# Performance work log

Hardware: AMD Instinct MI355X
Metric: run time of the kernel (lower is better)

## Reference

```python
import jax, jax.numpy as jnp
import numpy as np

B, A, T, C = 8, 16, 512, 256
H = 8
DH = C // H
HID = 4 * C


def setup_inputs() -> dict:
    key = jax.random.key(0)
    ks = jax.random.split(key, 16)
    s = 0.02
    return {
        "x": jax.random.normal(ks[0], (B, A, T, C), jnp.float32),
        "ln1_w": jnp.ones((C,), jnp.float32),
        "ln1_b": jnp.zeros((C,), jnp.float32),
        "qkv_w": jax.random.normal(ks[1], (C, 3 * C), jnp.float32) * s,
        "qkv_b": jnp.zeros((3 * C,), jnp.float32),
        "proj_w": jax.random.normal(ks[2], (C, C), jnp.float32) * s,
        "proj_b": jnp.zeros((C,), jnp.float32),
        "ln2_w": jnp.ones((C,), jnp.float32),
        "ln2_b": jnp.zeros((C,), jnp.float32),
        "fc_w": jax.random.normal(ks[3], (C, HID), jnp.float32) * s,
        "fc_b": jnp.zeros((HID,), jnp.float32),
        "fc2_w": jax.random.normal(ks[4], (HID, C), jnp.float32) * s,
        "fc2_b": jnp.zeros((C,), jnp.float32),
    }


def _layernorm(x, w, b, eps=1e-5):
    mu = jnp.mean(x, axis=-1, keepdims=True)
    var = jnp.var(x, axis=-1, keepdims=True)
    return (x - mu) * jax.lax.rsqrt(var + eps) * w + b


def reference(x, ln1_w, ln1_b, qkv_w, qkv_b, proj_w, proj_b,
              ln2_w, ln2_b, fc_w, fc_b, fc2_w, fc2_b):
    # pre-LN block; note: residuals branch off the *normalized* tensor,
    # exactly as in the source forward().
    xn = _layernorm(x, ln1_w, ln1_b)                       # (B,A,T,C)

    qkv = xn @ qkv_w + qkv_b                               # (B,A,T,3C)
    q, k, v = jnp.split(qkv, 3, axis=-1)
    # (B,A,T,C) -> (B,A,H,T,Dh)
    def heads(t):
        return t.reshape(B, A, T, H, DH).transpose(0, 1, 3, 2, 4)
    q, k, v = heads(q), heads(k), heads(v)

    att = jnp.einsum('bahtd,bahsd->bahts', q, k) / np.sqrt(DH).astype(np.float32)
    att = jax.nn.softmax(att, axis=-1)                     # (B,A,H,T,T)
    y = jnp.einsum('bahts,bahsd->bahtd', att, v)
    y = y.transpose(0, 1, 3, 2, 4).reshape(B, A, T, C)
    y = y @ proj_w + proj_b

    x2 = xn + y
    x2n = _layernorm(x2, ln2_w, ln2_b)
    h = jax.nn.gelu(x2n @ fc_w + fc_b, approximate=False)
    m = h @ fc2_w + fc2_b
    return x2n + m
```

## Files before the change

kernel.cpp:

```cpp
#include <hip/hip_runtime.h>

typedef unsigned short u16;
typedef __attribute__((ext_vector_type(8))) short s16x8;
typedef __attribute__((ext_vector_type(4))) float f32x4;

#define MFMA_BF16(a,b,c) __builtin_amdgcn_mfma_f32_16x16x32_bf16((a),(b),(c),0,0,0)

#define GLL(gp, lp) __builtin_amdgcn_global_load_lds( \
    (const __attribute__((address_space(1))) void*)(gp), \
    (__attribute__((address_space(3))) void*)(lp), 16, 0, 0)

#define PIPE_WAIT_BAR(N) do { \
  asm volatile("s_waitcnt vmcnt(" #N ")" ::: "memory"); \
  __builtin_amdgcn_sched_barrier(0); \
  __builtin_amdgcn_s_barrier(); \
  __builtin_amdgcn_sched_barrier(0); \
} while (0)

#define PIPE_BAR() do { \
  asm volatile("" ::: "memory"); \
  __builtin_amdgcn_sched_barrier(0); \
  __builtin_amdgcn_s_barrier(); \
  __builtin_amdgcn_sched_barrier(0); \
} while (0)

__device__ __forceinline__ float b2f(u16 s){
  union { unsigned u; float f; } v; v.u = ((unsigned)s) << 16; return v.f;
}
__device__ __forceinline__ u16 f2b(float x){
  union { float f; unsigned u; } v; v.f = x;
  unsigned u = v.u;
  return (u16)((u + 0x7FFFu + ((u >> 16) & 1u)) >> 16);
}
__device__ __forceinline__ u16 f2b_trunc(float x){
  union { float f; unsigned u; } v; v.f = x;
  return (u16)(v.u >> 16);
}

__device__ __forceinline__ float gelu_fast(float v){
  float av = fabsf(v) * 0.70710678118654752f;
  float t  = __builtin_amdgcn_rcpf(1.0f + 0.3275911f * av);
  float p  = ((((1.061405429f * t - 1.453152027f) * t + 1.421413741f) * t
               - 0.284496736f) * t + 0.254829592f) * t;
  float erfa = 1.0f - p * __expf(-av * av);
  return 0.5f * v * (1.0f + copysignf(erfa, v));
}

__global__ __launch_bounds__(256) void wconv_all(
    const float* __restrict__ w0, u16* __restrict__ t0,
    const float* __restrict__ w1, u16* __restrict__ t1,
    const float* __restrict__ w2, u16* __restrict__ t2,
    const float* __restrict__ w3, u16* __restrict__ t3)
{
  int bid = blockIdx.x;
  const float* w; u16* t; int K, N, base;
  if (bid < 768)        { w = w0; t = t0; K = 256;  N = 768;  base = bid; }
  else if (bid < 1024)  { w = w1; t = t1; K = 256;  N = 256;  base = bid - 768; }
  else if (bid < 2048)  { w = w2; t = t2; K = 256;  N = 1024; base = bid - 1024; }
  else                  { w = w3; t = t3; K = 1024; N = 256;  base = bid - 2048; }
  int idx = base * 256 + threadIdx.x;
  if (idx >= K * N) return;
  int k = idx / N, n = idx - k * N;
  t[(size_t)n * K + k] = f2b(w[idx]);
}

__global__ __launch_bounds__(256) void ln_f32(const float* __restrict__ in,
    const float* __restrict__ gam, const float* __restrict__ bet, u16* __restrict__ out)
{
  int wv = threadIdx.x >> 6, lane = threadIdx.x & 63;
  size_t row = (size_t)blockIdx.x * 4 + wv;
  float4 u = *(const float4*)(in + row * 256 + lane * 4);
  float s  = u.x + u.y + u.z + u.w;
  float s2 = u.x*u.x + u.y*u.y + u.z*u.z + u.w*u.w;
  #pragma unroll
  for (int off = 32; off; off >>= 1){
    s  += __shfl_xor(s, off);
    s2 += __shfl_xor(s2, off);
  }
  float mean = s * (1.0f/256.0f);
  float var  = s2 * (1.0f/256.0f) - mean*mean;
  float rs   = rsqrtf(var + 1e-5f);
  int c = lane * 4;
  float4 g4 = *(const float4*)(gam + c);
  float4 b4 = *(const float4*)(bet + c);
  ushort4 o;
  o.x = f2b((u.x - mean)*rs*g4.x + b4.x);
  o.y = f2b((u.y - mean)*rs*g4.y + b4.y);
  o.z = f2b((u.z - mean)*rs*g4.z + b4.z);
  o.w = f2b((u.w - mean)*rs*g4.w + b4.w);
  *(ushort4*)(out + row * 256 + c) = o;
}

template<int EPI, int NT>
__global__ __launch_bounds__(256) void gemm128(
    const u16* __restrict__ A, const u16* __restrict__ Bt, const float* __restrict__ bias,
    const u16* __restrict__ res, void* __restrict__ o0v, u16* __restrict__ o1, u16* __restrict__ o2,
    int N, int K)
{
  __shared__ __align__(16) u16 lds[24576];
  int tid = threadIdx.x;
  int w = tid >> 6, lane = tid & 63;
  int quad = lane >> 4, c = lane & 15;
  int bid = blockIdx.x;
  int x = bid & 7, j = bid >> 3;
  int nt = j % NT, mt = (j / NT) * 8 + x;
  int wm = (w >> 1) * 64, wn = (w & 1) * 64;
  const u16* Abase = A + (size_t)mt * 128 * K;
  const u16* Bbase = Bt + (size_t)nt * 128 * K;
  int m0 = tid & 127, jj0 = tid >> 7;
  f32x4 zero = {0.f, 0.f, 0.f, 0.f};
  f32x4 acc[4][4];
  #pragma unroll
  for (int mi = 0; mi < 4; mi++)
    #pragma unroll
    for (int ni = 0; ni < 4; ni++) acc[mi][ni] = zero;

  auto stage = [&](int buf, int k0){
    u16* base = &lds[buf * 8192];
    GLL(Abase + (size_t)m0 * K + k0 + jj0 * 8,       &base[tid * 8]);
    GLL(Abase + (size_t)m0 * K + k0 + (jj0 + 2) * 8, &base[2048 + tid * 8]);
    GLL(Bbase + (size_t)m0 * K + k0 + jj0 * 8,       &base[4096 + tid * 8]);
    GLL(Bbase + (size_t)m0 * K + k0 + (jj0 + 2) * 8, &base[6144 + tid * 8]);
  };
  auto compute = [&](int cb){
    const u16* Lb = &lds[cb * 8192];
    s16x8 af[4], bfr[4];
    #pragma unroll
    for (int mi = 0; mi < 4; mi++)
      af[mi] = *(const s16x8*)&Lb[(quad * 128 + wm + mi * 16 + c) * 8];
    #pragma unroll
    for (int ni = 0; ni < 4; ni++)
      bfr[ni] = *(const s16x8*)&Lb[4096 + (quad * 128 + wn + ni * 16 + c) * 8];
    #pragma unroll
    for (int mi = 0; mi < 4; mi++)
      #pragma unroll
      for (int ni = 0; ni < 4; ni++)
        acc[mi][ni] = MFMA_BF16(af[mi], bfr[ni], acc[mi][ni]);
  };

  stage(0, 0); stage(1, 32); stage(2, 64);
  int cur = 0;
  int k0 = 0;
  for (; k0 + 96 < K; k0 += 32){
    PIPE_WAIT_BAR(8);
    compute(cur);
    PIPE_BAR();
    stage(cur, k0 + 96);
    cur = (cur == 2) ? 0 : cur + 1;
  }
  PIPE_WAIT_BAR(8); compute(cur); cur = (cur == 2) ? 0 : cur + 1;
  PIPE_WAIT_BAR(4); compute(cur); cur = (cur == 2) ? 0 : cur + 1;
  PIPE_WAIT_BAR(0); compute(cur);

  const int LS  = 132;
  int rr = tid >> 3;
  int c7 = tid & 7;

  #pragma unroll
  for (int ch = 0; ch < 4; ch++){
    __syncthreads();
    if ((w >> 1) == (ch >> 1)){
      #pragma unroll
      for (int mi2 = 0; mi2 < 2; mi2++){
        int mi = (ch & 1) * 2 + mi2;
        #pragma unroll
        for (int ni = 0; ni < 4; ni++){
          int col = wn + ni * 16 + c;
          float bv = bias[nt * 128 + col];
          #pragma unroll
          for (int r = 0; r < 4; r++){
            int cr = mi2 * 16 + quad * 4 + r;
            float vv = acc[mi][ni][r] + bv;
            if (EPI == 0){
              int gcol = nt * 128 + col;
              if ((gcol >> 8) == 0) vv *= 0.17677669529663687f;
              lds[cr * LS + col] = f2b(vv);
            }
          }
        }
      }
    }
    __syncthreads();
    int row = mt * 128 + ch * 32 + rr;
    #pragma unroll
    for (int jj2 = 0; jj2 < 2; jj2++){
      int colL = c7 * 8 + jj2 * 64;
      uint4 val = *(const uint4*)&lds[rr * LS + colL];
      if (EPI == 0){
        int gcol = nt * 128 + colL;
        int which = gcol >> 8, ccc = gcol & 255;
        int hh = ccc >> 5, d = ccc & 31;
        int ba = row >> 9, t = row & 511;
        size_t idx = (((size_t)(ba * 8 + hh)) * 512 + t) * 32 + d;
        u16* dst = (which == 0) ? (u16*)o0v : ((which == 1) ? o1 : o2);
        *(uint4*)(dst + idx) = val;
      } else {
        *(uint4*)((u16*)o0v + (size_t)row * N + nt * 128 + colL) = val;
      }
    }
  }
}

__global__ __launch_bounds__(256) void ffn_fused(
    const u16* __restrict__ x2n, const u16* __restrict__ fcT, const float* __restrict__ fcb,
    const u16* __restrict__ fc2T, const float* __restrict__ fc2b, float* __restrict__ out)
{
  __shared__ __align__(16) u16 lds[24576];
  int tid = threadIdx.x;
  int w = tid >> 6, lane = tid & 63;
  int quad = lane >> 4, c = lane & 15;
  int mt = blockIdx.x;
  const u16* Abase = x2n + (size_t)mt * 64 * 256;
  char* ldsc = (char*)lds;
  char* hl   = (char*)lds + 32768;

  #pragma unroll
  for (int i = 0; i < 8; i++){
    int ci = i * 256 + tid;
    int row = ci >> 5, slot = ci & 31;
    int glow = (slot * 16) ^ ((row & 7) << 4);
    GLL((const char*)Abase + row * 512 + glow, ldsc + ci * 16);
  }
  f32x4 zero = {0.f, 0.f, 0.f, 0.f};
  f32x4 acc2[4][4];
  #pragma unroll
  for (int mi = 0; mi < 4; mi++)
    #pragma unroll
    for (int ni = 0; ni < 4; ni++) acc2[mi][ni] = zero;
  PIPE_WAIT_BAR(0);

  for (int hc = 0; hc < 8; hc++){
    f32x4 acc1[4][2];
    #pragma unroll
    for (int mi = 0; mi < 4; mi++){ acc1[mi][0] = zero; acc1[mi][1] = zero; }
    #pragma unroll
    for (int ks = 0; ks < 8; ks++){
      s16x8 af[4], bf1[2];
      #pragma unroll
      for (int ni = 0; ni < 2; ni++){
        int n = hc * 128 + w * 32 + ni * 16 + c;
        bf1[ni] = *(const s16x8*)(fcT + (size_t)n * 256 + ks * 32 + quad * 8);
      }
      #pragma unroll
      for (int mi = 0; mi < 4; mi++){
        int row = mi * 16 + c;
        int kb = (ks * 64 + quad * 16) ^ ((row & 7) << 4);
        af[mi] = *(const s16x8*)(ldsc + row * 512 + kb);
      }
      #pragma unroll
      for (int mi = 0; mi < 4; mi++){
        acc1[mi][0] = MFMA_BF16(af[mi], bf1[0], acc1[mi][0]);
        acc1[mi][1] = MFMA_BF16(af[mi], bf1[1], acc1[mi][1]);
      }
    }
    __syncthreads();
    #pragma unroll
    for (int ni = 0; ni < 2; ni++){
      int colc = w * 32 + ni * 16 + c;
      float bv = fcb[hc * 128 + colc];
      #pragma unroll
      for (int mi = 0; mi < 4; mi++){
        #pragma unroll
        for (int r = 0; r < 4; r++){
          int row = mi * 16 + quad * 4 + r;
          int by = (colc * 2) ^ ((row & 15) << 4);
          *(u16*)(hl + row * 256 + by) = f2b(gelu_fast(acc1[mi][ni][r] + bv));
        }
      }
    }
    __syncthreads();
    #pragma unroll
    for (int ks = 0; ks < 4; ks++){
      s16x8 ha[4], bf2[4];
      #pragma unroll
      for (int ni = 0; ni < 4; ni++){
        int n = w * 64 + ni * 16 + c;
        bf2[ni] = *(const s16x8*)(fc2T + (size_t)n * 1024 + hc * 128 + ks * 32 + quad * 8);
      }
      #pragma unroll
      for (int mi = 0; mi < 4; mi++){
        int row = mi * 16 + c;
        int kb = (ks * 64 + quad * 16) ^ ((row & 15) << 4);
        ha[mi] = *(const s16x8*)(hl + row * 256 + kb);
      }
      #pragma unroll
      for (int mi = 0; mi < 4; mi++)
        #pragma unroll
        for (int ni = 0; ni < 4; ni++)
          acc2[mi][ni] = MFMA_BF16(ha[mi], bf2[ni], acc2[mi][ni]);
    }
  }

  #pragma unroll
  for (int ni = 0; ni < 4; ni++){
    int col = w * 64 + ni * 16 + c;
    float bv = fc2b[col];
    #pragma unroll
    for (int mi = 0; mi < 4; mi++){
      #pragma unroll
      for (int r = 0; r < 4; r++){
        int row = mi * 16 + quad * 4 + r;
        int by = (col * 2) ^ ((row & 7) << 4);
        u16 xv = *(const u16*)(ldsc + row * 512 + by);
        acc2[mi][ni][r] += bv + b2f(xv);
      }
    }
  }
  __syncthreads();

  float* ldsF = (float*)lds;
  const int LSO = 260;
  int rr = tid >> 3, c8 = tid & 7;
  #pragma unroll
  for (int ch = 0; ch < 2; ch++){
    #pragma unroll
    for (int mi2 = 0; mi2 < 2; mi2++){
      int mi = ch * 2 + mi2;
      #pragma unroll
      for (int ni = 0; ni < 4; ni++){
        #pragma unroll
        for (int r = 0; r < 4; r++){
          int crow = mi2 * 16 + quad * 4 + r;
          ldsF[crow * LSO + w * 64 + ni * 16 + c] = acc2[mi][ni][r];
        }
      }
    }
    __syncthreads();
    size_t rb = ((size_t)mt * 64 + ch * 32 + rr) * 256;
    #pragma unroll
    for (int jj = 0; jj < 8; jj++){
      int col = c8 * 4 + jj * 32;
      *(float4*)(out + rb + col) = *(const float4*)&ldsF[rr * LSO + col];
    }
    __syncthreads();
  }
}

__global__ __launch_bounds__(256) void proj_ln(
    const u16* __restrict__ A, const u16* __restrict__ Bt, const float* __restrict__ bias,
    const u16* __restrict__ res, const float* __restrict__ gam, const float* __restrict__ bet,
    u16* __restrict__ x2n)
{
  __shared__ __align__(16) u16 lds[20480];
  int tid = threadIdx.x;
  int w = tid >> 6, lane = tid & 63;
  int quad = lane >> 4, c = lane & 15;
  int mt = blockIdx.x;
  int wn = w * 64;
  const u16* Abase = A + (size_t)mt * 64 * 256;
  int an = tid & 63, aj = tid >> 6;
  f32x4 zero = {0.f, 0.f, 0.f, 0.f};
  f32x4 acc[4][4];
  #pragma unroll
  for (int mi = 0; mi < 4; mi++)
    #pragma unroll
    for (int ni = 0; ni < 4; ni++) acc[mi][ni] = zero;

  auto stage = [&](int buf, int k0){
    u16* base = &lds[buf * 10240];
    GLL(Abase + (size_t)an * 256 + k0 + aj * 8, &base[tid * 8]);
    #pragma unroll
    for (int i = 0; i < 4; i++){
      int ci = tid + i * 256;
      int n = ci & 255, jjb = ci >> 8;
      GLL(Bt + (size_t)n * 256 + k0 + jjb * 8, &base[2048 + ci * 8]);
    }
  };
  auto compute = [&](int cb){
    const u16* base = &lds[cb * 10240];
    s16x8 af[4], bfr[4];
    #pragma unroll
    for (int mi = 0; mi < 4; mi++)
      af[mi] = *(const s16x8*)&base[(quad * 64 + mi * 16 + c) * 8];
    #pragma unroll
    for (int ni = 0; ni < 4; ni++)
      bfr[ni] = *(const s16x8*)&base[2048 + (quad * 256 + wn + ni * 16 + c) * 8];
    #pragma unroll
    for (int mi = 0; mi < 4; mi++)
      #pragma unroll
      for (int ni = 0; ni < 4; ni++)
        acc[mi][ni] = MFMA_BF16(af[mi], bfr[ni], acc[mi][ni]);
  };

  stage(0, 0);
  int cur = 0;
  for (int k0 = 32; k0 < 256; k0 += 32){
    stage(cur ^ 1, k0);
    PIPE_WAIT_BAR(5);
    compute(cur);
    PIPE_BAR();
    cur ^= 1;
  }
  PIPE_WAIT_BAR(0);
  compute(cur);
  __syncthreads();

  #pragma unroll
  for (int ni = 0; ni < 4; ni++){
    int col = wn + ni * 16 + c;
    float bv = bias[col];
    #pragma unroll
    for (int mi = 0; mi < 4; mi++){
      #pragma unroll
      for (int r = 0; r < 4; r++){
        int rowL = mi * 16 + quad * 4 + r;
        size_t gidx = ((size_t)mt * 64 + rowL) * 256 + col;
        lds[rowL * 264 + col] = f2b(acc[mi][ni][r] + bv + b2f(res[gidx]));
      }
    }
  }
  __syncthreads();

  int rowL = tid >> 2, part = (tid & 3) * 64;
  float s = 0.f, s2 = 0.f;
  #pragma unroll
  for (int i = 0; i < 16; i++){
    ushort4 u = *(const ushort4*)&lds[rowL * 264 + part + i * 4];
    float v0 = b2f(u.x), v1 = b2f(u.y), v2 = b2f(u.z), v3 = b2f(u.w);
    s  += v0 + v1 + v2 + v3;
    s2 += v0*v0 + v1*v1 + v2*v2 + v3*v3;
  }
  s  += __shfl_xor(s, 1);  s  += __shfl_xor(s, 2);
  s2 += __shfl_xor(s2, 1); s2 += __shfl_xor(s2, 2);
  float mean = s * (1.0f/256.0f);
  float var  = s2 * (1.0f/256.0f) - mean*mean;
  float rs   = rsqrtf(var + 1e-5f);
  size_t orow = ((size_t)mt * 64 + rowL) * 256;
  #pragma unroll
  for (int i = 0; i < 16; i++){
    int col = part + i * 4;
    ushort4 u = *(const ushort4*)&lds[rowL * 264 + col];
    float4 g4 = *(const float4*)(gam + col);
    float4 b4 = *(const float4*)(bet + col);
    ushort4 o;
    o.x = f2b((b2f(u.x) - mean)*rs*g4.x + b4.x);
    o.y = f2b((b2f(u.y) - mean)*rs*g4.y + b4.y);
    o.z = f2b((b2f(u.z) - mean)*rs*g4.z + b4.z);
    o.w = f2b((b2f(u.w) - mean)*rs*g4.w + b4.w);
    *(ushort4*)(x2n + orow + col) = o;
  }
}

__global__ __launch_bounds__(256) void attn_kernel(const u16* __restrict__ q,
    const u16* __restrict__ k, const u16* __restrict__ v, u16* __restrict__ y)
{
  __shared__ __align__(16) u16 ldsK[32 * 36];
  __shared__ __align__(16) u16 ldsV[32 * 36];
  __shared__ __align__(16) u16 ldsp[4][16 * 36];
  int tid = threadIdx.x;
  int w = tid >> 6, lane = tid & 63;
  int quad = lane >> 4, c = lane & 15;
  int bid = blockIdx.x;
  int x = bid & 7, j = bid >> 3;
  int qt = j & 3, bah = (j >> 2) * 8 + x;
  int q0 = qt * 128 + w * 32;
  const u16* qb = q + (size_t)bah * 16384;
  const u16* kb = k + (size_t)bah * 16384;
  const u16* vb = v + (size_t)bah * 16384;
  int krow = tid >> 3, kcol = (tid & 7) * 4;
  int vd = tid & 31,  vs = (tid >> 5) * 4;

  s16x8 qf0 = *(const s16x8*)(qb + (q0 + c) * 32 + quad * 8);
  s16x8 qf1 = *(const s16x8*)(qb + (q0 + 16 + c) * 32 + quad * 8);
  float l0[4] = {0.f,0.f,0.f,0.f}, l1[4] = {0.f,0.f,0.f,0.f};
  f32x4 o00 = {0,0,0,0}, o01 = {0,0,0,0}, o10 = {0,0,0,0}, o11 = {0,0,0,0};
  f32x4 zero = {0,0,0,0};

  for (int s0 = 0; s0 < 512; s0 += 32){
    uint2 kr = *(const uint2*)(kb + (s0 + krow) * 32 + kcol);
    short4 vr;
    vr.x = (short)vb[(s0 + vs)     * 32 + vd];
    vr.y = (short)vb[(s0 + vs + 1) * 32 + vd];
    vr.z = (short)vb[(s0 + vs + 2) * 32 + vd];
    vr.w = (short)vb[(s0 + vs + 3) * 32 + vd];
    __syncthreads();
    *(uint2*)&ldsK[krow * 36 + kcol] = kr;
    *(short4*)&ldsV[vd * 36 + vs]   = vr;
    __syncthreads();

    s16x8 kf0 = *(const s16x8*)&ldsK[c * 36 + quad * 8];
    s16x8 kf1 = *(const s16x8*)&ldsK[(16 + c) * 36 + quad * 8];
    s16x8 vf0 = *(const s16x8*)&ldsV[c * 36 + quad * 8];
    s16x8 vf1 = *(const s16x8*)&ldsV[(16 + c) * 36 + quad * 8];

    f32x4 S0 = MFMA_BF16(qf0, kf0, zero);
    f32x4 S1 = MFMA_BF16(qf0, kf1, zero);
    #pragma unroll
    for (int r = 0; r < 4; r++){
      float p0 = __expf(S0[r]), p1 = __expf(S1[r]);
      l0[r] += p0 + p1;
      int prow = quad * 4 + r;
      ldsp[w][prow * 36 + c]      = f2b_trunc(p0);
      ldsp[w][prow * 36 + 16 + c] = f2b_trunc(p1);
    }
    s16x8 pf = *(const s16x8*)&ldsp[w][c * 36 + quad * 8];
    o00 = MFMA_BF16(pf, vf0, o00);
    o01 = MFMA_BF16(pf, vf1, o01);

    S0 = MFMA_BF16(qf1, kf0, zero);
    S1 = MFMA_BF16(qf1, kf1, zero);
    #pragma unroll
    for (int r = 0; r < 4; r++){
      float p0 = __expf(S0[r]), p1 = __expf(S1[r]);
      l1[r] += p0 + p1;
      int prow = quad * 4 + r;
      ldsp[w][prow * 36 + c]      = f2b_trunc(p0);
      ldsp[w][prow * 36 + 16 + c] = f2b_trunc(p1);
    }
    pf = *(const s16x8*)&ldsp[w][c * 36 + quad * 8];
    o10 = MFMA_BF16(pf, vf0, o10);
    o11 = MFMA_BF16(pf, vf1, o11);
  }

  #pragma unroll
  for (int r = 0; r < 4; r++){
    #pragma unroll
    for (int off = 8; off; off >>= 1){
      l0[r] += __shfl_xor(l0[r], off);
      l1[r] += __shfl_xor(l1[r], off);
    }
  }

  int ba = bah >> 3, hh = bah & 7;
  #pragma unroll
  for (int r = 0; r < 4; r++){
    int t0 = q0 + quad * 4 + r;
    float inv0 = 1.0f / l0[r], inv1 = 1.0f / l1[r];
    size_t base0 = ((size_t)(ba * 512 + t0)) * 256 + hh * 32;
    size_t base1 = base0 + 16 * 256;
    y[base0 + c]      = f2b(o00[r] * inv0);
    y[base0 + 16 + c] = f2b(o01[r] * inv0);
    y[base1 + c]      = f2b(o10[r] * inv1);
    y[base1 + 16 + c] = f2b(o11[r] * inv1);
  }
}

extern "C" void kernel_launch(void* const* d_in, const int* in_sizes, int n_in,
                              void* d_out, int out_size, void* d_ws, size_t ws_size,
                              hipStream_t stream)
{
  const float* x      = (const float*)d_in[0];
  const float* ln1_w  = (const float*)d_in[1];
  const float* ln1_b  = (const float*)d_in[2];
  const float* qkv_w  = (const float*)d_in[3];
  const float* qkv_b  = (const float*)d_in[4];
  const float* proj_w = (const float*)d_in[5];
  const float* proj_b = (const float*)d_in[6];
  const float* ln2_w  = (const float*)d_in[7];
  const float* ln2_b  = (const float*)d_in[8];
  const float* fc_w   = (const float*)d_in[9];
  const float* fc_b   = (const float*)d_in[10];
  const float* fc2_w  = (const float*)d_in[11];
  const float* fc2_b  = (const float*)d_in[12];
  float* out = (float*)d_out;
  char* ws = (char*)d_ws;

  u16* xn   = (u16*)ws;
  u16* qb   = (u16*)(ws + (size_t)33554432);
  u16* kb   = qb + 16777216;
  u16* vb   = kb + 16777216;
  u16* yb   = vb + 16777216;
  u16* x2n  = (u16*)(ws + (size_t)173015040);
  u16* wqkvT  = (u16*)(ws + (size_t)206569472);
  u16* wprojT = wqkvT + 196608;
  u16* wfcT   = wprojT + 65536;
  u16* wfc2T  = wfcT + 262144;

  wconv_all<<<3072, 256, 0, stream>>>(qkv_w, wqkvT, proj_w, wprojT, fc_w, wfcT, fc2_w, wfc2T);

  ln_f32<<<16384, 256, 0, stream>>>(x, ln1_w, ln1_b, xn);
  gemm128<0,6><<<3072, 256, 0, stream>>>(xn, wqkvT, qkv_b, nullptr, qb, kb, vb, 768, 256);
  attn_kernel<<<4096, 256, 0, stream>>>(qb, kb, vb, yb);
  proj_ln<<<1024, 256, 0, stream>>>(yb, wprojT, proj_b, xn, ln2_w, ln2_b, x2n);
  ffn_fused<<<1024, 256, 0, stream>>>(x2n, wfcT, fc_b, wfc2T, fc2_b, out);
}
```

Measured before the change: 537.3 us.

## Split FFN fused kernel across eight waves instead of four

```diff
diff --git a/kernel.cpp b/kernel.cpp
--- a/kernel.cpp
+++ b/kernel.cpp
@@ -201,7 +201,7 @@
   }
 }
 
-__global__ __launch_bounds__(256) void ffn_fused(
+__global__ __launch_bounds__(512, 4) void ffn_fused(
     const u16* __restrict__ x2n, const u16* __restrict__ fcT, const float* __restrict__ fcb,
     const u16* __restrict__ fc2T, const float* __restrict__ fc2b, float* __restrict__ out)
 {
@@ -215,48 +215,38 @@
   char* hl   = (char*)lds + 32768;
 
   #pragma unroll
-  for (int i = 0; i < 8; i++){
-    int ci = i * 256 + tid;
+  for (int i = 0; i < 4; i++){
+    int ci = i * 512 + tid;
     int row = ci >> 5, slot = ci & 31;
     int glow = (slot * 16) ^ ((row & 7) << 4);
     GLL((const char*)Abase + row * 512 + glow, ldsc + ci * 16);
   }
   f32x4 zero = {0.f, 0.f, 0.f, 0.f};
-  f32x4 acc2[4][4];
-  #pragma unroll
-  for (int mi = 0; mi < 4; mi++)
-    #pragma unroll
-    for (int ni = 0; ni < 4; ni++) acc2[mi][ni] = zero;
+  f32x4 acc2[4][2];
+  #pragma unroll
+  for (int mi = 0; mi < 4; mi++){ acc2[mi][0] = zero; acc2[mi][1] = zero; }
   PIPE_WAIT_BAR(0);
 
   for (int hc = 0; hc < 8; hc++){
-    f32x4 acc1[4][2];
-    #pragma unroll
-    for (int mi = 0; mi < 4; mi++){ acc1[mi][0] = zero; acc1[mi][1] = zero; }
+    f32x4 acc1[4];
+    #pragma unroll
+    for (int mi = 0; mi < 4; mi++) acc1[mi] = zero;
+    int n1 = hc * 128 + w * 16 + c;
+    const u16* fb = fcT + (size_t)n1 * 256 + quad * 8;
     #pragma unroll
     for (int ks = 0; ks < 8; ks++){
-      s16x8 af[4], bf1[2];
-      #pragma unroll
-      for (int ni = 0; ni < 2; ni++){
-        int n = hc * 128 + w * 32 + ni * 16 + c;
-        bf1[ni] = *(const s16x8*)(fcT + (size_t)n * 256 + ks * 32 + quad * 8);
-      }
+      s16x8 bf1 = *(const s16x8*)(fb + ks * 32);
       #pragma unroll
       for (int mi = 0; mi < 4; mi++){
         int row = mi * 16 + c;
         int kb = (ks * 64 + quad * 16) ^ ((row & 7) << 4);
-        af[mi] = *(const s16x8*)(ldsc + row * 512 + kb);
-      }
-      #pragma unroll
-      for (int mi = 0; mi < 4; mi++){
-        acc1[mi][0] = MFMA_BF16(af[mi], bf1[0], acc1[mi][0]);
-        acc1[mi][1] = MFMA_BF16(af[mi], bf1[1], acc1[mi][1]);
-      }
-    }
-    __syncthreads();
-    #pragma unroll
-    for (int ni = 0; ni < 2; ni++){
-      int colc = w * 32 + ni * 16 + c;
+        s16x8 af = *(const s16x8*)(ldsc + row * 512 + kb);
+        acc1[mi] = MFMA_BF16(af, bf1, acc1[mi]);
+      }
+    }
+    __syncthreads();
+    {
+      int colc = w * 16 + c;
       float bv = fcb[hc * 128 + colc];
       #pragma unroll
       for (int mi = 0; mi < 4; mi++){
@@ -264,17 +254,17 @@
         for (int r = 0; r < 4; r++){
           int row = mi * 16 + quad * 4 + r;
           int by = (colc * 2) ^ ((row & 15) << 4);
-          *(u16*)(hl + row * 256 + by) = f2b(gelu_fast(acc1[mi][ni][r] + bv));
+          *(u16*)(hl + row * 256 + by) = f2b(gelu_fast(acc1[mi][r] + bv));
         }
       }
     }
     __syncthreads();
     #pragma unroll
     for (int ks = 0; ks < 4; ks++){
-      s16x8 ha[4], bf2[4];
-      #pragma unroll
-      for (int ni = 0; ni < 4; ni++){
-        int n = w * 64 + ni * 16 + c;
+      s16x8 ha[4], bf2[2];
+      #pragma unroll
+      for (int ni = 0; ni < 2; ni++){
+        int n = w * 32 + ni * 16 + c;
         bf2[ni] = *(const s16x8*)(fc2T + (size_t)n * 1024 + hc * 128 + ks * 32 + quad * 8);
       }
       #pragma unroll
@@ -284,16 +274,16 @@
         ha[mi] = *(const s16x8*)(hl + row * 256 + kb);
       }
       #pragma unroll
-      for (int mi = 0; mi < 4; mi++)
-        #pragma unroll
-        for (int ni = 0; ni < 4; ni++)
-          acc2[mi][ni] = MFMA_BF16(ha[mi], bf2[ni], acc2[mi][ni]);
-    }
-  }
-
-  #pragma unroll
-  for (int ni = 0; ni < 4; ni++){
-    int col = w * 64 + ni * 16 + c;
+      for (int mi = 0; mi < 4; mi++){
+        acc2[mi][0] = MFMA_BF16(ha[mi], bf2[0], acc2[mi][0]);
+        acc2[mi][1] = MFMA_BF16(ha[mi], bf2[1], acc2[mi][1]);
+      }
+    }
+  }
+
+  #pragma unroll
+  for (int ni = 0; ni < 2; ni++){
+    int col = w * 32 + ni * 16 + c;
     float bv = fc2b[col];
     #pragma unroll
     for (int mi = 0; mi < 4; mi++){
@@ -310,28 +300,21 @@
 
   float* ldsF = (float*)lds;
   const int LSO = 260;
-  int rr = tid >> 3, c8 = tid & 7;
-  #pragma unroll
-  for (int ch = 0; ch < 2; ch++){
-    #pragma unroll
-    for (int mi2 = 0; mi2 < 2; mi2++){
-      int mi = ch * 2 + mi2;
-      #pragma unroll
-      for (int ni = 0; ni < 4; ni++){
-        #pragma unroll
-        for (int r = 0; r < 4; r++){
-          int crow = mi2 * 16 + quad * 4 + r;
-          ldsF[crow * LSO + w * 64 + ni * 16 + c] = acc2[mi][ni][r];
-        }
-      }
-    }
-    __syncthreads();
-    size_t rb = ((size_t)mt * 64 + ch * 32 + rr) * 256;
-    #pragma unroll
-    for (int jj = 0; jj < 8; jj++){
-      int col = c8 * 4 + jj * 32;
-      *(float4*)(out + rb + col) = *(const float4*)&ldsF[rr * LSO + col];
-    }
+  int orow = tid >> 5, oc = (tid & 31) * 4;
+  #pragma unroll
+  for (int ch = 0; ch < 4; ch++){
+    #pragma unroll
+    for (int ni = 0; ni < 2; ni++){
+      #pragma unroll
+      for (int r = 0; r < 4; r++){
+        int crow = quad * 4 + r;
+        ldsF[crow * LSO + w * 32 + ni * 16 + c] = acc2[ch][ni][r];
+      }
+    }
+    __syncthreads();
+    size_t rb = ((size_t)mt * 64 + ch * 16 + orow) * 256;
+    *(float4*)(out + rb + oc)       = *(const float4*)&ldsF[orow * LSO + oc];
+    *(float4*)(out + rb + oc + 128) = *(const float4*)&ldsF[orow * LSO + oc + 128];
     __syncthreads();
   }
 }
@@ -572,5 +555,5 @@
   gemm128<0,6><<<3072, 256, 0, stream>>>(xn, wqkvT, qkv_b, nullptr, qb, kb, vb, 768, 256);
   attn_kernel<<<4096, 256, 0, stream>>>(qb, kb, vb, yb);
   proj_ln<<<1024, 256, 0, stream>>>(yb, wprojT, proj_b, xn, ln2_w, ln2_b, x2n);
-  ffn_fused<<<1024, 256, 0, stream>>>(x2n, wfcT, fc_b, wfc2T, fc2_b, out);
-}
+  ffn_fused<<<1024, 512, 0, stream>>>(x2n, wfcT, fc_b, wfc2T, fc2_b, out);
+}
```

Result: faster. 488.6 us (-9.1%).
